# Kernel tuning notes

Hardware: AMD Instinct MI355X
Metric: run time of the kernel (lower is better)

Reference implementation:

```python
import jax, jax.numpy as jnp
import numpy as np

D_MODEL = 1024
N_HEADS = 16
D_K = D_MODEL // N_HEADS
THETA = 10000.0
BATCH, SEQ = 2, 2048


def setup_inputs() -> dict:
    key = jax.random.key(0)
    k1, k2, k3 = jax.random.split(key, 3)
    std_qkv = float(np.sqrt(2.0 / (3 * D_MODEL + D_MODEL)))
    std_o = float(np.sqrt(2.0 / (D_MODEL + D_MODEL)))
    return {
        "x": jax.random.normal(k1, (BATCH, SEQ, D_MODEL), dtype=jnp.float32),
        "w_qkv": jax.random.normal(k2, (3 * D_MODEL, D_MODEL), dtype=jnp.float32) * std_qkv,
        "w_o": jax.random.normal(k3, (D_MODEL, D_MODEL), dtype=jnp.float32) * std_o,
        "token_positions": jnp.arange(SEQ, dtype=jnp.int32),
    }


def _rope(x, token_positions):
    # x: [..., s, d_k]; interleaved rotary embedding
    d_k = x.shape[-1]
    freqs = jnp.arange(0, d_k, 2, dtype=jnp.float32) / d_k          # [d_k/2]
    inv_freqs = 1.0 / (THETA ** freqs)
    angles = token_positions.astype(jnp.float32)[:, None] * inv_freqs  # [s, d_k/2]
    cos, sin = jnp.cos(angles), jnp.sin(angles)
    x_even, x_odd = x[..., 0::2], x[..., 1::2]
    rot_even = x_even * cos - x_odd * sin
    rot_odd = x_even * sin + x_odd * cos
    # interleave back: out[..., 2i] = rot_even[i], out[..., 2i+1] = rot_odd[i]
    return jnp.stack([rot_even, rot_odd], axis=-1).reshape(x.shape)


def reference(x, w_qkv, w_o, token_positions):
    b, s, _ = x.shape
    qkv = jnp.einsum('oi,bsi->bso', w_qkv, x)                        # [b, s, 3*d_model]
    q, k, v = jnp.split(qkv, 3, axis=-1)
    def to_heads(t):
        return t.reshape(b, s, N_HEADS, D_K).transpose(0, 2, 1, 3)  # [b, h, s, d]
    q, k, v = to_heads(q), to_heads(k), to_heads(v)
    q = _rope(q, token_positions)
    k = _rope(k, token_positions)
    scores = jnp.einsum('bhqd,bhkd->bhqk', q, k) / jnp.sqrt(jnp.float32(D_K))
    causal = jnp.tril(jnp.ones((s, s), dtype=bool))
    scores = jnp.where(causal, scores, -jnp.inf)
    attn = jax.nn.softmax(scores, axis=-1)
    y = jnp.einsum('bhqk,bhkd->bhqd', attn, v)
    y = y.transpose(0, 2, 1, 3).reshape(b, s, D_MODEL)
    return jnp.einsum('oi,bsi->bso', w_o, y)
```

## Files before the change

kernel.cpp:

```cpp
#include <hip/hip_runtime.h>
#include <math.h>

#define DEV __device__ __forceinline__

typedef __attribute__((ext_vector_type(8))) short bf16x8;
typedef __attribute__((ext_vector_type(4))) float f32x4;
typedef __attribute__((ext_vector_type(4))) unsigned int u32x4;

typedef __attribute__((address_space(3))) unsigned int lds_u32;
typedef const __attribute__((address_space(1))) unsigned int glb_u32;

DEV void gload16(const unsigned short* g, unsigned short* l) {
  __builtin_amdgcn_global_load_lds((glb_u32*)g, (lds_u32*)l, 16, 0, 0);
}

DEV bf16x8 lds_read8(const unsigned short* base, unsigned int byteoff) {
  return *reinterpret_cast<const bf16x8*>(
      reinterpret_cast<const char*>(base) + byteoff);
}

DEV float fexp2(float x) { return __builtin_amdgcn_exp2f(x); }

DEV unsigned short f2bf(float f) {
  union { float f; unsigned int u; } v; v.f = f;
  unsigned int u = v.u;
  unsigned int r = (u + 0x7fffu + ((u >> 16) & 1u)) >> 16;
  return (unsigned short)r;
}
DEV float bf2f(unsigned short h) {
  union { unsigned int u; float f; } v; v.u = ((unsigned int)h) << 16;
  return v.f;
}
DEV unsigned int cvtpk_bf16(float lo, float hi) {
  unsigned int r;
  asm("v_cvt_pk_bf16_f32 %0, %1, %2" : "=v"(r) : "v"(lo), "v"(hi));
  return r;
}

__global__ void cvt3_f32_bf16(const float* __restrict__ ina,
                              unsigned short* __restrict__ outa, int n4a,
                              const float* __restrict__ inb,
                              unsigned short* __restrict__ outb, int n4b,
                              const float* __restrict__ inc,
                              unsigned short* __restrict__ outc, int n4c) {
  int stride = gridDim.x * blockDim.x;
  int total = n4a + n4b + n4c;
  for (int i = blockIdx.x * blockDim.x + threadIdx.x; i < total; i += stride) {
    const float* src;
    unsigned short* dst;
    int j = i;
    if (j < n4a) {
      src = ina; dst = outa;
    } else if ((j -= n4a) < n4b) {
      src = inb; dst = outb;
    } else {
      j -= n4b; src = inc; dst = outc;
    }
    float4 f = reinterpret_cast<const float4*>(src)[j];
    ushort4 o;
    o.x = f2bf(f.x); o.y = f2bf(f.y); o.z = f2bf(f.z); o.w = f2bf(f.w);
    reinterpret_cast<ushort4*>(dst)[j] = o;
  }
}

__global__ __launch_bounds__(512, 2) void gemm8_qkv(const unsigned short* __restrict__ A,
                                                    const unsigned short* __restrict__ B,
                                                    unsigned short* __restrict__ C) {
  constexpr int K = 1024;
  constexpr int NK = 16;
  __shared__ unsigned short Ls[2][32768];

  const int tid = threadIdx.x;
  const int lane = tid & 63, wid = tid >> 6;
  const int wm = (wid >> 2) * 128;
  const int wn = (wid & 3) * 64;
  const int fr = lane & 15, kq = lane >> 4;

  int bid = blockIdx.x;
  int swz = (bid & 7) * 24 + (bid >> 3);
  int tm = swz & 15, tn = swz >> 4;
  const int arow0 = tm * 256, brow0 = tn * 256;

  const int subrow = lane >> 3;
  const int scol = ((lane & 7) ^ subrow) * 8;
  const unsigned short* aSrc = A + (size_t)(arow0 + wid * 8 + subrow) * K + scol;
  const unsigned short* bSrc = B + (size_t)(brow0 + wid * 8 + subrow) * K + scol;

  unsigned aoff[2], boff[2];
#pragma unroll
  for (int ks = 0; ks < 2; ks++) {
    unsigned x = ((unsigned)((ks * 4 + kq) ^ (fr & 7))) * 16;
    aoff[ks] = (unsigned)((wm + fr) * 128) + x;
    boff[ks] = 32768u + (unsigned)((wn + fr) * 128) + x;
  }

  f32x4 acc[8][4] = {};

#define STAGE_A8(BUF, H, T)                                                  \
  {                                                                          \
    gload16(aSrc + (size_t)((H) * 128) * K + (T) * 64,                       \
            &Ls[BUF][((H) * 128 + wid * 8) * 64]);                           \
    gload16(aSrc + (size_t)((H) * 128 + 64) * K + (T) * 64,                  \
            &Ls[BUF][((H) * 128 + 64 + wid * 8) * 64]);                      \
  }
#define STAGE_B8(BUF, H, T)                                                  \
  {                                                                          \
    gload16(bSrc + (size_t)((H) * 128) * K + (T) * 64,                       \
            &Ls[BUF][16384 + ((H) * 128 + wid * 8) * 64]);                   \
    gload16(bSrc + (size_t)((H) * 128 + 64) * K + (T) * 64,                  \
            &Ls[BUF][16384 + ((H) * 128 + 64 + wid * 8) * 64]);              \
  }

  STAGE_A8(0, 0, 0) STAGE_A8(0, 1, 0)
  STAGE_B8(0, 0, 0) STAGE_B8(0, 1, 0)
  STAGE_B8(1, 0, 1) STAGE_B8(1, 1, 1)
  asm volatile("s_waitcnt vmcnt(4)" ::: "memory");
  __builtin_amdgcn_s_barrier();

#define PHASE8(BUF, P, DO_STAGE)                                              \
  {                                                                           \
    bf16x8 af[2][2];                                                          \
    _Pragma("unroll") for (int mm = 0; mm < 2; mm++)                          \
      _Pragma("unroll") for (int ks = 0; ks < 2; ks++)                        \
        af[mm][ks] = lds_read8(Ls[BUF], aoff[ks] + ((P) * 2 + mm) * 2048);    \
    DO_STAGE                                                                  \
    __builtin_amdgcn_s_setprio(1);                                            \
    _Pragma("unroll") for (int mm = 0; mm < 2; mm++)                          \
      _Pragma("unroll") for (int j = 0; j < 4; j++)                           \
        _Pragma("unroll") for (int ks = 0; ks < 2; ks++)                      \
          acc[(P) * 2 + mm][j] = __builtin_amdgcn_mfma_f32_16x16x32_bf16(     \
              af[mm][ks], bq[j][ks], acc[(P) * 2 + mm][j], 0, 0, 0);          \
    __builtin_amdgcn_s_setprio(0);                                            \
  }

#define TILE8(T, BUF)                                                          \
  {                                                                            \
    bf16x8 bq[4][2];                                                           \
    _Pragma("unroll") for (int j = 0; j < 4; j++)                              \
      _Pragma("unroll") for (int ks = 0; ks < 2; ks++)                         \
        bq[j][ks] = lds_read8(Ls[BUF], boff[ks] + j * 2048);                   \
    PHASE8(BUF, 0, {                                                           \
      if ((T) + 1 < NK) { STAGE_A8(BUF ^ 1, 0, (T) + 1) STAGE_A8(BUF ^ 1, 1, (T) + 1) } \
    })                                                                         \
    __builtin_amdgcn_s_barrier();                                              \
    PHASE8(BUF, 1, { if ((T) + 2 < NK) STAGE_B8(BUF, 0, (T) + 2) })            \
    __builtin_amdgcn_s_barrier();                                              \
    PHASE8(BUF, 2, { if ((T) + 2 < NK) STAGE_B8(BUF, 1, (T) + 2) })            \
    __builtin_amdgcn_s_barrier();                                              \
    PHASE8(BUF, 3, {})                                                         \
    if ((T) + 2 < NK) {                                                        \
      asm volatile("s_waitcnt vmcnt(4)" ::: "memory");                         \
    } else {                                                                   \
      asm volatile("s_waitcnt vmcnt(0)" ::: "memory");                         \
    }                                                                          \
    __builtin_amdgcn_s_barrier();                                              \
    __builtin_amdgcn_sched_barrier(0);                                         \
  }

#pragma unroll 1
  for (int t = 0; t < NK; t += 2) {
    TILE8(t, 0)
    TILE8(t + 1, 1)
  }
#undef TILE8
#undef PHASE8
#undef STAGE_A8
#undef STAGE_B8

#pragma unroll
  for (int m = 0; m < 8; m++) {
#pragma unroll
    for (int j = 0; j < 4; j++) {
      size_t row = (size_t)(arow0 + wm + m * 16 + kq * 4);
      size_t col = (size_t)(brow0 + wn + j * 16 + fr);
#pragma unroll
      for (int r = 0; r < 4; r++)
        C[(row + r) * 3072 + col] = f2bf(acc[m][j][r]);
    }
  }
}

__global__ __launch_bounds__(256) void gemm_wo(const unsigned short* __restrict__ A,
                                               const unsigned short* __restrict__ B,
                                               float* __restrict__ C, int K) {
  __shared__ unsigned short Ab[2][4096];
  __shared__ unsigned short Bb[2][2048];
  const int tid = threadIdx.x;
  const int lane = tid & 63, wid = tid >> 6;
  const int wm = (wid >> 1) * 64, wn = (wid & 1) * 32;
  const int fr = lane & 15, kq = lane >> 4;
  const int arow0 = blockIdx.x * 128;
  const int brow0 = blockIdx.y * 64;

  const int srow = tid >> 2;
  const int schunk = (tid & 3) ^ (srow & 3);
  const unsigned short* aptr = A + (size_t)(arow0 + srow) * K + schunk * 8;
  const unsigned short* bptr = B + (size_t)(brow0 + srow) * K + schunk * 8;

  unsigned int offa[4], offb[2];
#pragma unroll
  for (int i = 0; i < 4; i++)
    offa[i] = (unsigned)((wm + i * 16 + fr) * 64 + ((kq ^ (fr & 3)) * 16));
#pragma unroll
  for (int j = 0; j < 2; j++)
    offb[j] = (unsigned)((wn + j * 16 + fr) * 64 + ((kq ^ (fr & 3)) * 16));

  f32x4 acc[4][2] = {};

#define WSTAGE(BI)                                                 \
  {                                                                \
    gload16(aptr, &Ab[BI][wid * 512]);                             \
    gload16(aptr + (size_t)64 * K, &Ab[BI][2048 + wid * 512]);     \
    gload16(bptr, &Bb[BI][wid * 512]);                             \
    aptr += 32;                                                    \
    bptr += 32;                                                    \
  }

#define WCOMP(BI)                                                                      \
  {                                                                                    \
    bf16x8 af[4], bfr[2];                                                              \
    _Pragma("unroll") for (int i = 0; i < 4; i++) af[i] = lds_read8(Ab[BI], offa[i]);  \
    _Pragma("unroll") for (int j = 0; j < 2; j++) bfr[j] = lds_read8(Bb[BI], offb[j]); \
    _Pragma("unroll") for (int i = 0; i < 4; i++)                                      \
      _Pragma("unroll") for (int j = 0; j < 2; j++)                                    \
        acc[i][j] = __builtin_amdgcn_mfma_f32_16x16x32_bf16(af[i], bfr[j], acc[i][j], 0, 0, 0); \
  }

  const int nk = K >> 5;
  WSTAGE(0);
  for (int ks = 0; ks < nk; ks += 2) {
    asm volatile("s_waitcnt lgkmcnt(0)" ::: "memory");
    __builtin_amdgcn_s_barrier();
    WSTAGE(1);
    asm volatile("s_waitcnt vmcnt(3)" ::: "memory");
    WCOMP(0);
    asm volatile("s_waitcnt lgkmcnt(0)" ::: "memory");
    __builtin_amdgcn_s_barrier();
    if (ks + 2 < nk) {
      WSTAGE(0);
      asm volatile("s_waitcnt vmcnt(3)" ::: "memory");
    } else {
      asm volatile("s_waitcnt vmcnt(0)" ::: "memory");
    }
    WCOMP(1);
  }
#undef WSTAGE
#undef WCOMP

#pragma unroll
  for (int i = 0; i < 4; i++) {
#pragma unroll
    for (int j = 0; j < 2; j++) {
#pragma unroll
      for (int r = 0; r < 4; r++) {
        size_t row = (size_t)(arow0 + wm + i * 16 + kq * 4 + r);
        size_t col = (size_t)(brow0 + wn + j * 16 + fr);
        C[row * 1024 + col] = acc[i][j][r];
      }
    }
  }
}

__global__ __launch_bounds__(256) void rope_vtrans_kernel(unsigned short* __restrict__ qkv,
                                                          const int* __restrict__ pos,
                                                          unsigned short* __restrict__ vt) {
  int bid0 = blockIdx.x;
  int t = threadIdx.x;
  if (bid0 < 4096) {
    int m = bid0;
    int s = m & 2047;
    __shared__ float Cl[32], Sl[32];
    if (t < 32) {
      float position = (float)pos[s];
      float inv = __expf(-(float)t * (9.210340371976184f / 32.0f));
      float ang = position * inv;
      Cl[t] = cosf(ang);
      Sl[t] = sinf(ang);
    }
    __syncthreads();
    const float QS = 0.18033688011112042f;
    int h = t >> 4, g = t & 15;
    float c0 = Cl[2 * g], s0 = Sl[2 * g], c1 = Cl[2 * g + 1], s1 = Sl[2 * g + 1];
    size_t base = (size_t)m * 3072 + h * 64 + 4 * g;
    ushort4 qv = *reinterpret_cast<ushort4*>(&qkv[base]);
    float qe0 = bf2f(qv.x), qo0 = bf2f(qv.y), qe1 = bf2f(qv.z), qo1 = bf2f(qv.w);
    qv.x = f2bf((qe0 * c0 - qo0 * s0) * QS);
    qv.y = f2bf((qe0 * s0 + qo0 * c0) * QS);
    qv.z = f2bf((qe1 * c1 - qo1 * s1) * QS);
    qv.w = f2bf((qe1 * s1 + qo1 * c1) * QS);
    *reinterpret_cast<ushort4*>(&qkv[base]) = qv;
    size_t kb = base + 1024;
    ushort4 kv = *reinterpret_cast<ushort4*>(&qkv[kb]);
    float ke0 = bf2f(kv.x), ko0 = bf2f(kv.y), ke1 = bf2f(kv.z), ko1 = bf2f(kv.w);
    kv.x = f2bf(ke0 * c0 - ko0 * s0);
    kv.y = f2bf(ke0 * s0 + ko0 * c0);
    kv.z = f2bf(ke1 * c1 - ko1 * s1);
    kv.w = f2bf(ke1 * s1 + ko1 * c1);
    *reinterpret_cast<ushort4*>(&qkv[kb]) = kv;
  } else {
    int bid = bid0 - 4096;
    int sb = bid & 31;
    int bh = bid >> 5;
    int h = bh & 15, b = bh >> 4;
    __shared__ unsigned short tile[64][72];
    int sl = t >> 2, c0 = (t & 3) * 16;
    const unsigned short* src = qkv + (size_t)(b * 2048 + sb * 64) * 3072 + 2048 + h * 64;
    *reinterpret_cast<bf16x8*>(&tile[sl][c0]) =
        *reinterpret_cast<const bf16x8*>(&src[(size_t)sl * 3072 + c0]);
    *reinterpret_cast<bf16x8*>(&tile[sl][c0 + 8]) =
        *reinterpret_cast<const bf16x8*>(&src[(size_t)sl * 3072 + c0 + 8]);
    __syncthreads();
    int d = t >> 2, p0 = (t & 3) * 16;
    unsigned short* dst = vt + ((size_t)bh * 64 + d) * 2048 + sb * 64 + p0;
    bf16x8 o0, o1;
#pragma unroll
    for (int i = 0; i < 8; i++) {
      int p = p0 + i;
      int s_in = (p & 32) + ((p >> 2) & 1) * 16 + ((p >> 3) & 3) * 4 + (p & 3);
      o0[i] = (short)tile[s_in][d];
    }
#pragma unroll
    for (int i = 0; i < 8; i++) {
      int p = p0 + 8 + i;
      int s_in = (p & 32) + ((p >> 2) & 1) * 16 + ((p >> 3) & 3) * 4 + (p & 3);
      o1[i] = (short)tile[s_in][d];
    }
    *reinterpret_cast<bf16x8*>(dst) = o0;
    *reinterpret_cast<bf16x8*>(dst + 8) = o1;
  }
}

__global__ __launch_bounds__(256, 4) void attn_kernel(const unsigned short* __restrict__ qkv,
                                                      const unsigned short* __restrict__ vt,
                                                      unsigned short* __restrict__ Y) {
  int bid = blockIdx.x;
  int g = bid & 255;
  int r = bid >> 8;
  int bh = g & 31;
  int t0 = g >> 5;
  int qt = (r == 0) ? t0 : (r == 1) ? (15 - t0) : (r == 2) ? (16 + t0) : (31 - t0);
  int h = bh & 15, b = bh >> 4;
  int tid = threadIdx.x, lane = tid & 63, wid = tid >> 6;
  int fr = lane & 15, kq = lane >> 4;
  int qbase = qt * 64 + wid * 16;

  const size_t mrow0 = (size_t)b * 2048;
  const unsigned short* Qp = qkv + (mrow0 + qbase) * 3072 + h * 64;
  const unsigned short* Kp = qkv + mrow0 * 3072 + 1024 + h * 64;
  const unsigned short* Vp = vt + ((size_t)bh * 64) * 2048;

  __shared__ unsigned short Klds[2][4096];
  __shared__ unsigned short Vlds[2][4096];

  bf16x8 qf[2];
#pragma unroll
  for (int ks = 0; ks < 2; ks++)
    qf[ks] = *reinterpret_cast<const bf16x8*>(&Qp[(size_t)fr * 3072 + ks * 32 + kq * 8]);

  const int srow = tid >> 3;
  const int schunk = (tid & 7) ^ (srow & 7);
  const unsigned short* kstage = Kp + (size_t)srow * 3072 + schunk * 8;
  const unsigned short* vstage = Vp + (size_t)srow * 2048 + schunk * 8;

  unsigned int offk[8], offv[8];
#pragma unroll
  for (int gg = 0; gg < 4; gg++)
#pragma unroll
    for (int ks = 0; ks < 2; ks++) {
      int R = gg * 16 + fr;
      offk[gg * 2 + ks] = (unsigned)(R * 128 + (((4 * ks + kq) ^ (R & 7)) * 16));
    }
#pragma unroll
  for (int db = 0; db < 4; db++)
#pragma unroll
    for (int hf = 0; hf < 2; hf++) {
      int d = db * 16 + fr;
      offv[db * 2 + hf] = (unsigned)(d * 128 + (((4 * hf + kq) ^ (d & 7)) * 16));
    }

  bf16x8 vones;
#pragma unroll
  for (int i = 0; i < 8; i++) vones[i] = (short)0x3F80;

  f32x4 acc[4] = {};
  f32x4 lacc = {};
  const int q_lane = qbase + fr;
  const int ntiles = qt + 1;

#define STAGE(BI)                                                     \
  {                                                                   \
    gload16(kstage, &Klds[BI][wid * 512]);                            \
    gload16(kstage + (size_t)32 * 3072, &Klds[BI][2048 + wid * 512]); \
    gload16(vstage, &Vlds[BI][wid * 512]);                            \
    gload16(vstage + 32 * 2048, &Vlds[BI][2048 + wid * 512]);         \
    kstage += (size_t)64 * 3072;                                      \
    vstage += 64;                                                     \
  }

#define TILE_COMPUTE(T, BI)                                                           \
  {                                                                                   \
    const bool masked_ = ((T) == qt);                                                 \
    f32x4 sc[4] = {};                                                                 \
    __builtin_amdgcn_s_setprio(1);                                                    \
    _Pragma("unroll") for (int gg = 0; gg < 4; gg++) {                                \
      _Pragma("unroll") for (int ks = 0; ks < 2; ks++) {                              \
        bf16x8 kf = lds_read8(Klds[BI], offk[gg * 2 + ks]);                           \
        sc[gg] = __builtin_amdgcn_mfma_f32_16x16x32_bf16(kf, qf[ks], sc[gg], 0, 0, 0);\
      }                                                                               \
    }                                                                                 \
    __builtin_amdgcn_s_setprio(0);                                                    \
    float p[16];                                                                      \
    _Pragma("unroll") for (int gg = 0; gg < 4; gg++)                                  \
      _Pragma("unroll") for (int rr = 0; rr < 4; rr++) {                              \
        float v = sc[gg][rr];                                                         \
        if (masked_) {                                                                \
          int k = (T) * 64 + gg * 16 + kq * 4 + rr;                                   \
          if (k > q_lane) v = -1e30f;                                                 \
        }                                                                             \
        p[gg * 4 + rr] = fexp2(v);                                                    \
      }                                                                               \
    u32x4 W0 = {cvtpk_bf16(p[0], p[1]), cvtpk_bf16(p[2], p[3]),                       \
                cvtpk_bf16(p[4], p[5]), cvtpk_bf16(p[6], p[7])};                      \
    u32x4 W1 = {cvtpk_bf16(p[8], p[9]), cvtpk_bf16(p[10], p[11]),                     \
                cvtpk_bf16(p[12], p[13]), cvtpk_bf16(p[14], p[15])};                  \
    bf16x8 pa0 = *reinterpret_cast<bf16x8*>(&W0);                                     \
    bf16x8 pa1 = *reinterpret_cast<bf16x8*>(&W1);                                     \
    __builtin_amdgcn_s_setprio(1);                                                    \
    _Pragma("unroll") for (int db = 0; db < 4; db++) {                                \
      bf16x8 vf0 = lds_read8(Vlds[BI], offv[db * 2]);                                 \
      acc[db] = __builtin_amdgcn_mfma_f32_16x16x32_bf16(vf0, pa0, acc[db], 0, 0, 0);  \
      bf16x8 vf1 = lds_read8(Vlds[BI], offv[db * 2 + 1]);                             \
      acc[db] = __builtin_amdgcn_mfma_f32_16x16x32_bf16(vf1, pa1, acc[db], 0, 0, 0);  \
    }                                                                                 \
    lacc = __builtin_amdgcn_mfma_f32_16x16x32_bf16(vones, pa0, lacc, 0, 0, 0);        \
    lacc = __builtin_amdgcn_mfma_f32_16x16x32_bf16(vones, pa1, lacc, 0, 0, 0);        \
    __builtin_amdgcn_s_setprio(0);                                                    \
  }

  STAGE(0);
  for (int t = 0; t < ntiles; t += 2) {
    asm volatile("s_waitcnt lgkmcnt(0)" ::: "memory");
    __builtin_amdgcn_s_barrier();
    if (t + 1 < ntiles) {
      STAGE(1);
      asm volatile("s_waitcnt vmcnt(4)" ::: "memory");
    } else {
      asm volatile("s_waitcnt vmcnt(0)" ::: "memory");
    }
    TILE_COMPUTE(t, 0);
    if (t + 1 >= ntiles) break;
    asm volatile("s_waitcnt lgkmcnt(0)" ::: "memory");
    __builtin_amdgcn_s_barrier();
    if (t + 2 < ntiles) {
      STAGE(0);
      asm volatile("s_waitcnt vmcnt(4)" ::: "memory");
    } else {
      asm volatile("s_waitcnt vmcnt(0)" ::: "memory");
    }
    TILE_COMPUTE(t + 1, 1);
  }
#undef TILE_COMPUTE
#undef STAGE

  float inv = 1.0f / lacc[0];
  unsigned short* yp = Y + (mrow0 + qbase + fr) * 1024 + h * 64 + kq * 4;
#pragma unroll
  for (int db = 0; db < 4; db++) {
    ushort4 o;
    o.x = f2bf(acc[db][0] * inv);
    o.y = f2bf(acc[db][1] * inv);
    o.z = f2bf(acc[db][2] * inv);
    o.w = f2bf(acc[db][3] * inv);
    *reinterpret_cast<ushort4*>(yp + db * 16) = o;
  }
}

extern "C" void kernel_launch(void* const* d_in, const int* in_sizes, int n_in,
                              void* d_out, int out_size, void* d_ws, size_t ws_size,
                              hipStream_t stream) {
  const float* x     = (const float*)d_in[0];
  const float* w_qkv = (const float*)d_in[1];
  const float* w_o   = (const float*)d_in[2];
  const int*   pos   = (const int*)d_in[3];
  float* out = (float*)d_out;

  unsigned char* ws = (unsigned char*)d_ws;
  unsigned short* x_bf    = (unsigned short*)(ws);
  unsigned short* wqkv_bf = (unsigned short*)(ws + 8388608);
  unsigned short* wo_bf   = (unsigned short*)(ws + 14680064);
  unsigned short* qkv     = (unsigned short*)(ws + 16777216);
  unsigned short* vt      = (unsigned short*)(ws + 41943040);
  unsigned short* y       = (unsigned short*)(ws + 50331648);

  cvt3_f32_bf16<<<1536, 256, 0, stream>>>(x, x_bf, 4096 * 1024 / 4,
                                          w_qkv, wqkv_bf, 3072 * 1024 / 4,
                                          w_o, wo_bf, 1024 * 1024 / 4);

  gemm8_qkv<<<192, 512, 0, stream>>>(x_bf, wqkv_bf, qkv);

  rope_vtrans_kernel<<<5120, 256, 0, stream>>>(qkv, pos, vt);

  attn_kernel<<<1024, 256, 0, stream>>>(qkv, vt, y);

  gemm_wo<<<dim3(32, 16), 256, 0, stream>>>(y, wo_bf, out, 1024);
}
```

Measured before the change: 109.3 us.

## Split long causal query tiles across two blocks and add combine kernel

Rebalances causal attention work. Each block now processes either the first 16 key tiles of a long query tile (31-pair), or the remaining key tiles of that tile plus the short query tile (pair). The two halves of a long tile write unnormalized bf16 partial outputs and row sums into reused workspace, and a new attn_combine kernel sums them and normalizes. This evens out per-block work so fewer blocks sit idle in the tail, at the cost of an extra launch, partial-result traffic, and rounding the partials to bf16 before they are combined.

After: 104.3 us. 4.6% less time.

```diff
diff --git a/kernel.cpp b/kernel.cpp
--- a/kernel.cpp
+++ b/kernel.cpp
@@ -332,35 +332,26 @@
 
 __global__ __launch_bounds__(256, 4) void attn_kernel(const unsigned short* __restrict__ qkv,
                                                       const unsigned short* __restrict__ vt,
-                                                      unsigned short* __restrict__ Y) {
+                                                      unsigned short* __restrict__ Y,
+                                                      unsigned short* __restrict__ Opart,
+                                                      float* __restrict__ Lsum) {
   int bid = blockIdx.x;
-  int g = bid & 255;
-  int r = bid >> 8;
-  int bh = g & 31;
-  int t0 = g >> 5;
-  int qt = (r == 0) ? t0 : (r == 1) ? (15 - t0) : (r == 2) ? (16 + t0) : (31 - t0);
+  int bh = bid & 31;
+  int pair = (bid >> 5) & 15;
+  int halfsel = bid >> 9;
   int h = bh & 15, b = bh >> 4;
   int tid = threadIdx.x, lane = tid & 63, wid = tid >> 6;
   int fr = lane & 15, kq = lane >> 4;
-  int qbase = qt * 64 + wid * 16;
 
   const size_t mrow0 = (size_t)b * 2048;
-  const unsigned short* Qp = qkv + (mrow0 + qbase) * 3072 + h * 64;
   const unsigned short* Kp = qkv + mrow0 * 3072 + 1024 + h * 64;
   const unsigned short* Vp = vt + ((size_t)bh * 64) * 2048;
 
   __shared__ unsigned short Klds[2][4096];
   __shared__ unsigned short Vlds[2][4096];
 
-  bf16x8 qf[2];
-#pragma unroll
-  for (int ks = 0; ks < 2; ks++)
-    qf[ks] = *reinterpret_cast<const bf16x8*>(&Qp[(size_t)fr * 3072 + ks * 32 + kq * 8]);
-
   const int srow = tid >> 3;
   const int schunk = (tid & 7) ^ (srow & 7);
-  const unsigned short* kstage = Kp + (size_t)srow * 3072 + schunk * 8;
-  const unsigned short* vstage = Vp + (size_t)srow * 2048 + schunk * 8;
 
   unsigned int offk[8], offv[8];
 #pragma unroll
@@ -381,11 +372,6 @@
   bf16x8 vones;
 #pragma unroll
   for (int i = 0; i < 8; i++) vones[i] = (short)0x3F80;
-
-  f32x4 acc[4] = {};
-  f32x4 lacc = {};
-  const int q_lane = qbase + fr;
-  const int ntiles = qt + 1;
 
 #define STAGE(BI)                                                     \
   {                                                                   \
@@ -399,7 +385,7 @@
 
 #define TILE_COMPUTE(T, BI)                                                           \
   {                                                                                   \
-    const bool masked_ = ((T) == qt);                                                 \
+    const bool masked_ = ((T) == qt_);                                                \
     f32x4 sc[4] = {};                                                                 \
     __builtin_amdgcn_s_setprio(1);                                                    \
     _Pragma("unroll") for (int gg = 0; gg < 4; gg++) {                                \
@@ -415,7 +401,7 @@
         float v = sc[gg][rr];                                                         \
         if (masked_) {                                                                \
           int k = (T) * 64 + gg * 16 + kq * 4 + rr;                                   \
-          if (k > q_lane) v = -1e30f;                                                 \
+          if (k > q_lane_) v = -1e30f;                                                \
         }                                                                             \
         p[gg * 4 + rr] = fexp2(v);                                                    \
       }                                                                               \
@@ -437,42 +423,255 @@
     __builtin_amdgcn_s_setprio(0);                                                    \
   }
 
-  STAGE(0);
-  for (int t = 0; t < ntiles; t += 2) {
-    asm volatile("s_waitcnt lgkmcnt(0)" ::: "memory");
+#define ATTN_RANGE(QT_, TLO_, THI_, MODE_, HALF_)                                     \
+  {                                                                                   \
+    const int qt_ = (QT_);                                                            \
+    const int qbase_ = qt_ * 64 + wid * 16;                                           \
+    const int q_lane_ = qbase_ + fr;                                                  \
+    const unsigned short* Qp = qkv + (mrow0 + qbase_) * 3072 + h * 64;                \
+    bf16x8 qf[2];                                                                     \
+    _Pragma("unroll") for (int ks = 0; ks < 2; ks++)                                  \
+      qf[ks] = *reinterpret_cast<const bf16x8*>(                                      \
+          &Qp[(size_t)fr * 3072 + ks * 32 + kq * 8]);                                 \
+    const unsigned short* kstage =                                                    \
+        Kp + (size_t)srow * 3072 + schunk * 8 + (size_t)(TLO_) * 64 * 3072;           \
+    const unsigned short* vstage =                                                    \
+        Vp + (size_t)srow * 2048 + schunk * 8 + (TLO_) * 64;                          \
+    f32x4 acc[4] = {};                                                                \
+    f32x4 lacc = {};                                                                  \
+    const int nt_ = (THI_) - (TLO_);                                                  \
+    STAGE(0);                                                                         \
+    for (int u = 0; u < nt_; u += 2) {                                                \
+      asm volatile("s_waitcnt lgkmcnt(0)" ::: "memory");                              \
+      __builtin_amdgcn_s_barrier();                                                   \
+      if (u + 1 < nt_) {                                                              \
+        STAGE(1);                                                                     \
+        asm volatile("s_waitcnt vmcnt(4)" ::: "memory");                              \
+      } else {                                                                        \
+        asm volatile("s_waitcnt vmcnt(0)" ::: "memory");                              \
+      }                                                                               \
+      TILE_COMPUTE((TLO_) + u, 0);                                                    \
+      if (u + 1 >= nt_) break;                                                        \
+      asm volatile("s_waitcnt lgkmcnt(0)" ::: "memory");                              \
+      __builtin_amdgcn_s_barrier();                                                   \
+      if (u + 2 < nt_) {                                                              \
+        STAGE(0);                                                                     \
+        asm volatile("s_waitcnt vmcnt(4)" ::: "memory");                              \
+      } else {                                                                        \
+        asm volatile("s_waitcnt vmcnt(0)" ::: "memory");                              \
+      }                                                                               \
+      TILE_COMPUTE((TLO_) + u + 1, 1);                                                \
+    }                                                                                 \
+    if (MODE_ == 0) {                                                                 \
+      float inv = 1.0f / lacc[0];                                                     \
+      unsigned short* yp = Y + (mrow0 + qbase_ + fr) * 1024 + h * 64 + kq * 4;        \
+      _Pragma("unroll") for (int db = 0; db < 4; db++) {                              \
+        ushort4 o;                                                                    \
+        o.x = f2bf(acc[db][0] * inv);                                                 \
+        o.y = f2bf(acc[db][1] * inv);                                                 \
+        o.z = f2bf(acc[db][2] * inv);                                                 \
+        o.w = f2bf(acc[db][3] * inv);                                                 \
+        *reinterpret_cast<ushort4*>(yp + db * 16) = o;                                \
+      }                                                                               \
+    } else {                                                                          \
+      const int slot = (pair * 2 + (HALF_)) * 32 + bh;                                \
+      unsigned short* op = Opart + (size_t)slot * 4096;                               \
+      _Pragma("unroll") for (int db = 0; db < 4; db++)                                \
+        _Pragma("unroll") for (int rr = 0; rr < 4; rr++) {                            \
+          int d = db * 16 + kq * 4 + rr;                                              \
+          op[(wid * 16 + 0) * 0 + d * 64 + (qbase_ & 63) + fr - (qbase_ & 63)] =      \
+              f2bf(acc[db][rr]);                                                      \
+        }                                                                             \
+      if (kq == 0) Lsum[slot * 256 + wid * 16 + 0 * 64 + (fr) + wid * 0] = lacc[0];   \
+    }                                                                                 \
+  }
+
+
+  if (halfsel == 0) {
+    const int Lt = 31 - pair;
+    {
+      const int qt_ = Lt;
+      const int qbase_ = qt_ * 64 + wid * 16;
+      const int q_lane_ = qbase_ + fr;
+      const unsigned short* Qp = qkv + (mrow0 + qbase_) * 3072 + h * 64;
+      bf16x8 qf[2];
+#pragma unroll
+      for (int ks = 0; ks < 2; ks++)
+        qf[ks] = *reinterpret_cast<const bf16x8*>(&Qp[(size_t)fr * 3072 + ks * 32 + kq * 8]);
+      const unsigned short* kstage = Kp + (size_t)srow * 3072 + schunk * 8;
+      const unsigned short* vstage = Vp + (size_t)srow * 2048 + schunk * 8;
+      f32x4 acc[4] = {};
+      f32x4 lacc = {};
+      const int nt_ = 16;
+      STAGE(0);
+      for (int u = 0; u < nt_; u += 2) {
+        asm volatile("s_waitcnt lgkmcnt(0)" ::: "memory");
+        __builtin_amdgcn_s_barrier();
+        if (u + 1 < nt_) {
+          STAGE(1);
+          asm volatile("s_waitcnt vmcnt(4)" ::: "memory");
+        } else {
+          asm volatile("s_waitcnt vmcnt(0)" ::: "memory");
+        }
+        TILE_COMPUTE(u, 0);
+        if (u + 1 >= nt_) break;
+        asm volatile("s_waitcnt lgkmcnt(0)" ::: "memory");
+        __builtin_amdgcn_s_barrier();
+        if (u + 2 < nt_) {
+          STAGE(0);
+          asm volatile("s_waitcnt vmcnt(4)" ::: "memory");
+        } else {
+          asm volatile("s_waitcnt vmcnt(0)" ::: "memory");
+        }
+        TILE_COMPUTE(u + 1, 1);
+      }
+      const int slot = (pair * 2 + 0) * 32 + bh;
+      unsigned short* op = Opart + (size_t)slot * 4096;
+      int qcol = wid * 16 + fr;
+#pragma unroll
+      for (int db = 0; db < 4; db++)
+#pragma unroll
+        for (int rr = 0; rr < 4; rr++) {
+          int d = db * 16 + kq * 4 + rr;
+          op[d * 64 + qcol] = f2bf(acc[db][rr]);
+        }
+      if (kq == 0) Lsum[slot * 64 + qcol] = lacc[0];
+    }
+  } else {
+    const int Lt = 31 - pair;
+    {
+      const int qt_ = Lt;
+      const int qbase_ = qt_ * 64 + wid * 16;
+      const int q_lane_ = qbase_ + fr;
+      const unsigned short* Qp = qkv + (mrow0 + qbase_) * 3072 + h * 64;
+      bf16x8 qf[2];
+#pragma unroll
+      for (int ks = 0; ks < 2; ks++)
+        qf[ks] = *reinterpret_cast<const bf16x8*>(&Qp[(size_t)fr * 3072 + ks * 32 + kq * 8]);
+      const unsigned short* kstage = Kp + (size_t)srow * 3072 + schunk * 8 + (size_t)16 * 64 * 3072;
+      const unsigned short* vstage = Vp + (size_t)srow * 2048 + schunk * 8 + 16 * 64;
+      f32x4 acc[4] = {};
+      f32x4 lacc = {};
+      const int nt_ = 16 - pair;
+      STAGE(0);
+      for (int u = 0; u < nt_; u += 2) {
+        asm volatile("s_waitcnt lgkmcnt(0)" ::: "memory");
+        __builtin_amdgcn_s_barrier();
+        if (u + 1 < nt_) {
+          STAGE(1);
+          asm volatile("s_waitcnt vmcnt(4)" ::: "memory");
+        } else {
+          asm volatile("s_waitcnt vmcnt(0)" ::: "memory");
+        }
+        TILE_COMPUTE(16 + u, 0);
+        if (u + 1 >= nt_) break;
+        asm volatile("s_waitcnt lgkmcnt(0)" ::: "memory");
+        __builtin_amdgcn_s_barrier();
+        if (u + 2 < nt_) {
+          STAGE(0);
+          asm volatile("s_waitcnt vmcnt(4)" ::: "memory");
+        } else {
+          asm volatile("s_waitcnt vmcnt(0)" ::: "memory");
+        }
+        TILE_COMPUTE(16 + u + 1, 1);
+      }
+      const int slot = (pair * 2 + 1) * 32 + bh;
+      unsigned short* op = Opart + (size_t)slot * 4096;
+      int qcol = wid * 16 + fr;
+#pragma unroll
+      for (int db = 0; db < 4; db++)
+#pragma unroll
+        for (int rr = 0; rr < 4; rr++) {
+          int d = db * 16 + kq * 4 + rr;
+          op[d * 64 + qcol] = f2bf(acc[db][rr]);
+        }
+      if (kq == 0) Lsum[slot * 64 + qcol] = lacc[0];
+    }
+    asm volatile("s_waitcnt lgkmcnt(0) vmcnt(0)" ::: "memory");
     __builtin_amdgcn_s_barrier();
-    if (t + 1 < ntiles) {
-      STAGE(1);
-      asm volatile("s_waitcnt vmcnt(4)" ::: "memory");
-    } else {
-      asm volatile("s_waitcnt vmcnt(0)" ::: "memory");
-    }
-    TILE_COMPUTE(t, 0);
-    if (t + 1 >= ntiles) break;
-    asm volatile("s_waitcnt lgkmcnt(0)" ::: "memory");
-    __builtin_amdgcn_s_barrier();
-    if (t + 2 < ntiles) {
+    {
+      const int qt_ = pair;
+      const int qbase_ = qt_ * 64 + wid * 16;
+      const int q_lane_ = qbase_ + fr;
+      const unsigned short* Qp = qkv + (mrow0 + qbase_) * 3072 + h * 64;
+      bf16x8 qf[2];
+#pragma unroll
+      for (int ks = 0; ks < 2; ks++)
+        qf[ks] = *reinterpret_cast<const bf16x8*>(&Qp[(size_t)fr * 3072 + ks * 32 + kq * 8]);
+      const unsigned short* kstage = Kp + (size_t)srow * 3072 + schunk * 8;
+      const unsigned short* vstage = Vp + (size_t)srow * 2048 + schunk * 8;
+      f32x4 acc[4] = {};
+      f32x4 lacc = {};
+      const int nt_ = pair + 1;
       STAGE(0);
-      asm volatile("s_waitcnt vmcnt(4)" ::: "memory");
-    } else {
-      asm volatile("s_waitcnt vmcnt(0)" ::: "memory");
-    }
-    TILE_COMPUTE(t + 1, 1);
-  }
+      for (int u = 0; u < nt_; u += 2) {
+        asm volatile("s_waitcnt lgkmcnt(0)" ::: "memory");
+        __builtin_amdgcn_s_barrier();
+        if (u + 1 < nt_) {
+          STAGE(1);
+          asm volatile("s_waitcnt vmcnt(4)" ::: "memory");
+        } else {
+          asm volatile("s_waitcnt vmcnt(0)" ::: "memory");
+        }
+        TILE_COMPUTE(u, 0);
+        if (u + 1 >= nt_) break;
+        asm volatile("s_waitcnt lgkmcnt(0)" ::: "memory");
+        __builtin_amdgcn_s_barrier();
+        if (u + 2 < nt_) {
+          STAGE(0);
+          asm volatile("s_waitcnt vmcnt(4)" ::: "memory");
+        } else {
+          asm volatile("s_waitcnt vmcnt(0)" ::: "memory");
+        }
+        TILE_COMPUTE(u + 1, 1);
+      }
+      float inv = 1.0f / lacc[0];
+      unsigned short* yp = Y + (mrow0 + qbase_ + fr) * 1024 + h * 64 + kq * 4;
+#pragma unroll
+      for (int db = 0; db < 4; db++) {
+        ushort4 o;
+        o.x = f2bf(acc[db][0] * inv);
+        o.y = f2bf(acc[db][1] * inv);
+        o.z = f2bf(acc[db][2] * inv);
+        o.w = f2bf(acc[db][3] * inv);
+        *reinterpret_cast<ushort4*>(yp + db * 16) = o;
+      }
+    }
+  }
+#undef ATTN_RANGE
 #undef TILE_COMPUTE
 #undef STAGE
-
-  float inv = 1.0f / lacc[0];
-  unsigned short* yp = Y + (mrow0 + qbase + fr) * 1024 + h * 64 + kq * 4;
-#pragma unroll
-  for (int db = 0; db < 4; db++) {
-    ushort4 o;
-    o.x = f2bf(acc[db][0] * inv);
-    o.y = f2bf(acc[db][1] * inv);
-    o.z = f2bf(acc[db][2] * inv);
-    o.w = f2bf(acc[db][3] * inv);
-    *reinterpret_cast<ushort4*>(yp + db * 16) = o;
-  }
+}
+
+__global__ __launch_bounds__(256) void attn_combine(const unsigned short* __restrict__ Opart,
+                                                    const float* __restrict__ Lsum,
+                                                    unsigned short* __restrict__ Y) {
+  int bid = blockIdx.x;
+  int pair = bid >> 5;
+  int bh = bid & 31;
+  int Lt = 31 - pair;
+  int h = bh & 15, b = bh >> 4;
+  int t = threadIdx.x;
+  int q = t >> 2, d0 = (t & 3) * 16;
+  size_t s0 = (size_t)((pair * 2 + 0) * 32 + bh);
+  size_t s1 = (size_t)((pair * 2 + 1) * 32 + bh);
+  float inv = 1.0f / (Lsum[s0 * 64 + q] + Lsum[s1 * 64 + q]);
+  const unsigned short* p0 = Opart + s0 * 4096;
+  const unsigned short* p1 = Opart + s1 * 4096;
+  bf16x8 o0, o1;
+#pragma unroll
+  for (int i = 0; i < 8; i++) {
+    int d = d0 + i;
+    o0[i] = (short)f2bf((bf2f(p0[d * 64 + q]) + bf2f(p1[d * 64 + q])) * inv);
+  }
+#pragma unroll
+  for (int i = 0; i < 8; i++) {
+    int d = d0 + 8 + i;
+    o1[i] = (short)f2bf((bf2f(p0[d * 64 + q]) + bf2f(p1[d * 64 + q])) * inv);
+  }
+  unsigned short* yp = Y + ((size_t)(b * 2048 + Lt * 64 + q)) * 1024 + h * 64 + d0;
+  *reinterpret_cast<bf16x8*>(yp) = o0;
+  *reinterpret_cast<bf16x8*>(yp + 8) = o1;
 }
 
 extern "C" void kernel_launch(void* const* d_in, const int* in_sizes, int n_in,
@@ -491,6 +690,8 @@
   unsigned short* qkv     = (unsigned short*)(ws + 16777216);
   unsigned short* vt      = (unsigned short*)(ws + 41943040);
   unsigned short* y       = (unsigned short*)(ws + 50331648);
+  unsigned short* Opart = x_bf;
+  float* Lsum = (float*)wqkv_bf;
 
   cvt3_f32_bf16<<<1536, 256, 0, stream>>>(x, x_bf, 4096 * 1024 / 4,
                                           w_qkv, wqkv_bf, 3072 * 1024 / 4,
@@ -500,7 +701,8 @@
 
   rope_vtrans_kernel<<<5120, 256, 0, stream>>>(qkv, pos, vt);
 
-  attn_kernel<<<1024, 256, 0, stream>>>(qkv, vt, y);
+  attn_kernel<<<1024, 256, 0, stream>>>(qkv, vt, y, Opart, Lsum);
+  attn_combine<<<512, 256, 0, stream>>>(Opart, Lsum, y);
 
   gemm_wo<<<dim3(32, 16), 256, 0, stream>>>(y, wo_bf, out, 1024);
 }
```
